# Optimization experiments

Measured on AMD Instinct MI355X. Metric: run time of the kernel, lower is better.

## Reference

```python
import jax, jax.numpy as jnp
import numpy as np

EPS = 1e-5
H = 12  # num_heads

def ste_sign(x):
    # forward: sign(x) in {-1,+1}; backward: grad passes where |x|<1 (clip STE)
    c = jnp.clip(x, -1.0, 1.0)
    s = jnp.where(x >= 0, 1.0, -1.0).astype(x.dtype)
    return c + jax.lax.stop_gradient(s - c)

def bin_w(w):
    # adaptive per-output-channel scaling: alpha = mean|w| (detached), weight = alpha*sign(w)
    alpha = jax.lax.stop_gradient(jnp.mean(jnp.abs(w), axis=1, keepdims=True))
    return alpha * ste_sign(w)

def layernorm(x, g, b):
    mu = jnp.mean(x, axis=-1, keepdims=True)
    var = jnp.var(x, axis=-1, keepdims=True)
    return (x - mu) * jax.lax.rsqrt(var + EPS) * g + b

def setup_inputs():
    key = jax.random.key(0)
    ks = jax.random.split(key, 6)
    B, N, C, hid = 8, 1024, 768, 3072
    s = 0.02
    return {
        "x": jax.random.normal(ks[0], (B, N, C), jnp.float32),
        "ln1_g": jnp.ones((C,), jnp.float32),
        "ln1_b": jnp.zeros((C,), jnp.float32),
        "w_qkv": jax.random.normal(ks[1], (3 * C, C), jnp.float32) * s,
        "w_proj": jax.random.normal(ks[2], (C, C), jnp.float32) * s,
        "b_proj": jnp.zeros((C,), jnp.float32),
        "ls1_g": 1e-5 * jnp.ones((C,), jnp.float32),
        "ln2_g": jnp.ones((C,), jnp.float32),
        "ln2_b": jnp.zeros((C,), jnp.float32),
        "w_fc1": jax.random.normal(ks[3], (hid, C), jnp.float32) * s,
        "b_fc1": jnp.zeros((hid,), jnp.float32),
        "w_fc2": jax.random.normal(ks[4], (C, hid), jnp.float32) * s,
        "b_fc2": jnp.zeros((C,), jnp.float32),
        "ls2_g": 1e-5 * jnp.ones((C,), jnp.float32),
    }

def reference(x, ln1_g, ln1_b, w_qkv, w_proj, b_proj, ls1_g, ln2_g, ln2_b, w_fc1, b_fc1, w_fc2, b_fc2, ls2_g):
    B, N, C = x.shape
    hd = C // H
    scale = hd ** -0.5
    # --- binarized attention ---
    h = layernorm(x, ln1_g, ln1_b)
    qkv = jnp.einsum('bnc,oc->bno', ste_sign(h), bin_w(w_qkv))        # 1w1a qkv proj
    qkv = qkv.reshape(B, N, 3, H, hd).transpose(2, 0, 3, 1, 4)        # [3,B,H,N,hd]
    bqkv = ste_sign(qkv)                                              # BinaryQuantizer
    q, k, v = bqkv[0], bqkv[1], bqkv[2]
    attn = jnp.einsum('bhnd,bhmd->bhnm', q, k) * scale                # [B,H,N,N]
    sm = jax.nn.softmax(attn, axis=-1)
    abin = (attn > 0).astype(x.dtype)                                 # SoftmaxBinaryQuantizer fwd value
    attn_eff = sm + jax.lax.stop_gradient(abin - sm)                  # STE: fwd=binary, bwd=softmax
    o = jnp.einsum('bhnm,bhmd->bhnd', attn_eff, v)
    o = o.transpose(0, 2, 1, 3).reshape(B, N, C)
    o = jnp.einsum('bnc,oc->bno', ste_sign(o), bin_w(w_proj)) + b_proj
    x = x + ls1_g * o
    # --- binary MLP (1-bit weight, 32-bit activation) ---
    h2 = layernorm(x, ln2_g, ln2_b)
    m = jax.nn.gelu(jnp.einsum('bnc,hc->bnh', h2, bin_w(w_fc1)) + b_fc1, approximate=False)
    m = jnp.einsum('bnh,ch->bnc', m, bin_w(w_fc2)) + b_fc2
    return x + ls2_g * m
```

## Files before the change

kernel.cpp:

```cpp
#include <hip/hip_runtime.h>

#define NTOK 8192
#define CDIM 768
#define HIDD 3072
#define NQKV 2304
#define SEQL 1024
#define NHEAD 12

typedef int i32x4 __attribute__((ext_vector_type(4)));
typedef float f32x4 __attribute__((ext_vector_type(4)));
typedef signed char sc16 __attribute__((ext_vector_type(16)));
typedef unsigned short us4 __attribute__((ext_vector_type(4)));

__device__ __forceinline__ unsigned short f32_to_bf16(float f) {
    unsigned int u = __float_as_uint(f);
    u += 0x7FFFu + ((u >> 16) & 1u);
    return (unsigned short)(u >> 16);
}
__device__ __forceinline__ float bf16_to_f32(unsigned short h) {
    return __uint_as_float(((unsigned)h) << 16);
}

__device__ __forceinline__ void gload_lds16(const void* g, void* l) {
    __builtin_amdgcn_global_load_lds(
        (const __attribute__((address_space(1))) unsigned int*)g,
        (__attribute__((address_space(3))) unsigned int*)l, 16, 0, 0);
}

__global__ void __launch_bounds__(256) prep_all(
    const float* __restrict__ w_proj, const float* __restrict__ w_fc1,
    const float* __restrict__ w_fc2,  const float* __restrict__ w_qkv,
    signed char* __restrict__ wproj_s, signed char* __restrict__ wfc1_s,
    signed char* __restrict__ wfc2_s,  signed char* __restrict__ wqkv_s,
    float* __restrict__ a_proj, float* __restrict__ a_fc1, float* __restrict__ a_fc2,
    const float* __restrict__ x, const float* __restrict__ ln1_g,
    const float* __restrict__ ln1_b, signed char* __restrict__ a1)
{
    const int blk = blockIdx.x;
    __shared__ float red[8];

    if (blk >= 6912) {
        int row = blk - 6912;
        const float* xr = x + (size_t)row * CDIM;
        float v0 = xr[threadIdx.x], v1 = xr[threadIdx.x + 256], v2 = xr[threadIdx.x + 512];
        float s = v0 + v1 + v2, s2 = v0 * v0 + v1 * v1 + v2 * v2;
        for (int off = 32; off > 0; off >>= 1) { s += __shfl_down(s, off); s2 += __shfl_down(s2, off); }
        if ((threadIdx.x & 63) == 0) { red[threadIdx.x >> 6] = s; red[4 + (threadIdx.x >> 6)] = s2; }
        __syncthreads();
        float ts = red[0] + red[1] + red[2] + red[3];
        float t2 = red[4] + red[5] + red[6] + red[7];
        float mu = ts * (1.0f / CDIM);
        float var = t2 * (1.0f / CDIM) - mu * mu;
        float rstd = rsqrtf(var + 1e-5f);
        signed char* orow = a1 + (size_t)row * CDIM;
        float vv[3] = {v0, v1, v2};
#pragma unroll
        for (int p = 0; p < 3; p++) {
            int i = threadIdx.x + p * 256;
            float val = (vv[p] - mu) * rstd * ln1_g[i] + ln1_b[i];
            orow[i] = (val >= 0.f) ? 1 : -1;
        }
        return;
    }

    const float* w; signed char* ws; float* alpha; int K; bool perm; int row;
    if (blk < 768)       { w = w_proj; ws = wproj_s; alpha = a_proj; K = CDIM; perm = true;  row = blk; }
    else if (blk < 3840) { w = w_fc1;  ws = wfc1_s;  alpha = a_fc1;  K = CDIM; perm = false; row = blk - 768; }
    else if (blk < 4608) { w = w_fc2;  ws = wfc2_s;  alpha = a_fc2;  K = HIDD; perm = true;  row = blk - 3840; }
    else                 { w = w_qkv;  ws = wqkv_s;  alpha = nullptr; K = CDIM; perm = false; row = blk - 4608; }

    const float* wr = w + (size_t)row * K;
    signed char* wsr = ws + (size_t)row * K;
    float s = 0.f;
    for (int i = threadIdx.x; i < K; i += 256) {
        float v = wr[i];
        int ip = perm ? ((i & ~63) | (((i & 15) << 2) | ((i >> 4) & 3))) : i;
        wsr[ip] = (v >= 0.f) ? 1 : -1;
        s += fabsf(v);
    }
    if (alpha) {
        for (int off = 32; off > 0; off >>= 1) s += __shfl_down(s, off);
        if ((threadIdx.x & 63) == 0) red[threadIdx.x >> 6] = s;
        __syncthreads();
        if (threadIdx.x == 0) alpha[row] = (red[0] + red[1] + red[2] + red[3]) / (float)K;
    }
}

__global__ void __launch_bounds__(256) ln2q_kernel(const unsigned short* __restrict__ x, const float* __restrict__ g,
                                                   const float* __restrict__ b, signed char* __restrict__ out,
                                                   float* __restrict__ rowscale) {
    int row = blockIdx.x;
    const unsigned short* xr = x + (size_t)row * CDIM;
    float v0 = bf16_to_f32(xr[threadIdx.x]);
    float v1 = bf16_to_f32(xr[threadIdx.x + 256]);
    float v2 = bf16_to_f32(xr[threadIdx.x + 512]);
    float s = v0 + v1 + v2, s2 = v0 * v0 + v1 * v1 + v2 * v2;
    for (int off = 32; off > 0; off >>= 1) { s += __shfl_down(s, off); s2 += __shfl_down(s2, off); }
    __shared__ float red[8];
    __shared__ float redm[4];
    if ((threadIdx.x & 63) == 0) { red[threadIdx.x >> 6] = s; red[4 + (threadIdx.x >> 6)] = s2; }
    __syncthreads();
    float ts = red[0] + red[1] + red[2] + red[3];
    float t2 = red[4] + red[5] + red[6] + red[7];
    float mu = ts * (1.0f / CDIM);
    float var = t2 * (1.0f / CDIM) - mu * mu;
    float rstd = rsqrtf(var + 1e-5f);
    float a0 = (v0 - mu) * rstd * g[threadIdx.x] + b[threadIdx.x];
    float a1 = (v1 - mu) * rstd * g[threadIdx.x + 256] + b[threadIdx.x + 256];
    float a2v = (v2 - mu) * rstd * g[threadIdx.x + 512] + b[threadIdx.x + 512];
    float mx = fmaxf(fabsf(a0), fmaxf(fabsf(a1), fabsf(a2v)));
    for (int off = 32; off > 0; off >>= 1) mx = fmaxf(mx, __shfl_down(mx, off));
    if ((threadIdx.x & 63) == 0) redm[threadIdx.x >> 6] = mx;
    __syncthreads();
    float rmax = fmaxf(fmaxf(redm[0], redm[1]), fmaxf(redm[2], redm[3]));
    rmax = fmaxf(rmax, 1e-20f);
    float inv = 127.f / rmax;
    signed char* orow = out + (size_t)row * CDIM;
    orow[threadIdx.x]       = (signed char)__float2int_rn(a0 * inv);
    orow[threadIdx.x + 256] = (signed char)__float2int_rn(a1 * inv);
    orow[threadIdx.x + 512] = (signed char)__float2int_rn(a2v * inv);
    if (threadIdx.x == 0) rowscale[row] = rmax * (1.f / 127.f);
}

enum { EPI_GELU = 2, EPI_QKV = 3 };
#define MSCALE_INV 16.0f

template<int EPI>
__global__ void __launch_bounds__(512, 4) gemm_i8(
    const signed char* __restrict__ A, const signed char* __restrict__ B,
    int M, int N, int K,
    const float* __restrict__ alpha, const float* __restrict__ bias,
    const float* __restrict__ rowscale,
    signed char* __restrict__ outB, signed char* __restrict__ vtB)
{
    __shared__ __align__(16) char lds_raw[3 * (256 + 128) * 64];
    auto As = (signed char (*)[256][64])lds_raw;
    auto Bs = (signed char (*)[128][64])(lds_raw + 3 * 256 * 64);

    const int tid = threadIdx.x, ln = tid & 63, w = tid >> 6;
    const int wm = w >> 1, wn = w & 1;
    const int lq = ln & 15, khi = ln >> 4;

    const int nwg = gridDim.x * gridDim.y;
    const int id = blockIdx.y * gridDim.x + blockIdx.x;
    const int nid = (id & 7) * (nwg >> 3) + (id >> 3);
    const int bxs = nid % gridDim.x, bys = nid / gridDim.x;
    const int bm = bys * 256, bn = bxs * 128;

    const i32x4 iz = {0, 0, 0, 0};
    i32x4 acc[4][4];
#pragma unroll
    for (int m = 0; m < 4; m++)
#pragma unroll
        for (int n = 0; n < 4; n++) acc[m][n] = iz;

    const int srow = tid >> 2, scol = (tid & 3) * 16;
    const int ssrc = ((tid & 3) ^ ((srow >> 1) & 3)) * 16;
    const int sa = 16 * (khi ^ ((lq >> 1) & 3));

    auto STAGE = [&](int p, int k0) {
        gload_lds16(A + (size_t)(bm + srow) * K + k0 + ssrc, &As[p][srow][scol]);
        gload_lds16(A + (size_t)(bm + 128 + srow) * K + k0 + ssrc, &As[p][128 + srow][scol]);
        gload_lds16(B + (size_t)(bn + srow) * K + k0 + ssrc, &Bs[p][srow][scol]);
    };
    auto COMPUTE = [&](int p, bool prefetch, int knext) {
        i32x4 aF[4], bF[4];
#pragma unroll
        for (int m = 0; m < 4; m++) aF[m] = *(const i32x4*)&As[p][wm * 64 + m * 16 + lq][sa];
#pragma unroll
        for (int n = 0; n < 4; n++) bF[n] = *(const i32x4*)&Bs[p][wn * 64 + n * 16 + lq][sa];
        if (prefetch) STAGE((p + 2) % 3, knext);
        __builtin_amdgcn_s_setprio(1);
#pragma unroll
        for (int m = 0; m < 4; m++)
#pragma unroll
            for (int n = 0; n < 4; n++)
                acc[m][n] = __builtin_amdgcn_mfma_i32_16x16x64_i8(aF[m], bF[n], acc[m][n], 0, 0, 0);
        __builtin_amdgcn_s_setprio(0);
    };

    const int nst = K >> 6;
    STAGE(0, 0);
    STAGE(1, 64);
#pragma unroll 1
    for (int t = 0; t < nst - 1; t++) {
        asm volatile("s_waitcnt vmcnt(3)" ::: "memory");
        asm volatile("s_waitcnt lgkmcnt(0)" ::: "memory");
        __builtin_amdgcn_s_barrier();
        COMPUTE(t % 3, t + 2 < nst, (t + 2) << 6);
    }
    asm volatile("s_waitcnt vmcnt(0)" ::: "memory");
    asm volatile("s_waitcnt lgkmcnt(0)" ::: "memory");
    __builtin_amdgcn_s_barrier();
    COMPUTE((nst - 1) % 3, false, 0);

    const int r0 = bm + wm * 64;
    const int c0 = bn + wn * 64;

    if constexpr (EPI == EPI_GELU) {
        float al[4], bi[4];
#pragma unroll
        for (int n = 0; n < 4; n++) {
            al[n] = alpha[c0 + n * 16 + lq];
            bi[n] = bias[c0 + n * 16 + lq];
        }
#pragma unroll
        for (int m = 0; m < 4; m++)
#pragma unroll
            for (int i = 0; i < 4; i++) {
                int r = r0 + m * 16 + khi * 4 + i;
                float rs = rowscale[r];
                unsigned pk = 0;
#pragma unroll
                for (int n = 0; n < 4; n++) {
                    float t = al[n] * ((float)acc[m][n][i] * rs) + bi[n];
                    float y2 = 1.5957691f * t + 0.07135481f * t * t * t;
                    float ge = t * __builtin_amdgcn_rcpf(1.0f + __expf(-y2));
                    float qf = fminf(fmaxf(ge * MSCALE_INV, -127.f), 127.f);
                    pk |= (unsigned)(unsigned char)(signed char)__float2int_rn(qf) << (8 * n);
                }
                *(unsigned*)(outB + (size_t)r * N + c0 + lq * 4) = pk;
            }
    } else {
        if (c0 < 1536) {
#pragma unroll
            for (int m = 0; m < 4; m++)
#pragma unroll
                for (int i = 0; i < 4; i++) {
                    int r = r0 + m * 16 + khi * 4 + i;
                    unsigned pk = 0;
#pragma unroll
                    for (int n = 0; n < 4; n++)
                        pk |= (unsigned)(unsigned char)(signed char)((acc[m][n][i] >= 0) ? 1 : -1) << (8 * n);
                    *(unsigned*)(outB + (size_t)r * 1536 + c0 + lq * 4) = pk;
                }
        } else {
#pragma unroll
            for (int m = 0; m < 4; m++)
#pragma unroll
                for (int n = 0; n < 4; n++) {
                    int cg = c0 + n * 16 + lq - 1536;
                    int hh = cg >> 6, dd = cg & 63;
                    int rb = r0 + m * 16 + khi * 4;
                    unsigned pk = 0;
#pragma unroll
                    for (int i = 0; i < 4; i++)
                        pk |= (unsigned)(unsigned char)(signed char)((acc[m][n][i] >= 0) ? 1 : -1) << (8 * i);
                    *(unsigned*)(vtB + (((size_t)(rb >> 10) * NHEAD + hh) * 64 + dd) * SEQL + (rb & 1023)) = pk;
                }
        }
    }
}

template<bool FINAL>
__global__ void __launch_bounds__(256) gemm_resid(
    const signed char* __restrict__ A, const signed char* __restrict__ B,
    int N, int K,
    const float* __restrict__ alpha, const float* __restrict__ bias,
    const float* __restrict__ ls,
    const float* __restrict__ residF, const unsigned short* __restrict__ residH,
    float ascale,
    float* __restrict__ outF, unsigned short* __restrict__ outH)
{
    __shared__ __align__(16) char lds_raw[3 * (128 + 64) * 64];
    auto As = (signed char (*)[128][64])lds_raw;
    auto Bs = (signed char (*)[64][64])(lds_raw + 3 * 128 * 64);

    const int tid = threadIdx.x, ln = tid & 63, w = tid >> 6;
    const int wm = w >> 1, wn = w & 1;
    const int lq = ln & 15, khi = ln >> 4;

    const int nwg = gridDim.x * gridDim.y;
    const int id = blockIdx.y * gridDim.x + blockIdx.x;
    const int nid = (id & 7) * (nwg >> 3) + (id >> 3);
    const int bxs = nid % gridDim.x, bys = nid / gridDim.x;
    const int bm = bys * 128, bn = bxs * 64;

    const int erow = tid >> 4;
    const int ec4 = (tid & 15) * 4;
    f32x4 a4 = *(const f32x4*)&alpha[bn + ec4];
    f32x4 b4 = *(const f32x4*)&bias[bn + ec4];
    f32x4 l4 = *(const f32x4*)&ls[bn + ec4];
    f32x4 rF[8];
    us4 rH[8];
#pragma unroll
    for (int p = 0; p < 8; p++) {
        size_t g = (size_t)(bm + p * 16 + erow) * N + bn + ec4;
        if constexpr (FINAL) rH[p] = *(const us4*)&residH[g];
        else                 rF[p] = *(const f32x4*)&residF[g];
    }

    const i32x4 iz = {0, 0, 0, 0};
    i32x4 acc[4][2];
#pragma unroll
    for (int m = 0; m < 4; m++)
#pragma unroll
        for (int n = 0; n < 2; n++) acc[m][n] = iz;

    const int srow = tid >> 2, scol = (tid & 3) * 16;
    const int ssrc = ((tid & 3) ^ ((srow >> 1) & 3)) * 16;
    const int sa = 16 * (khi ^ ((lq >> 1) & 3));

    auto STAGE = [&](int p, int k0) {
        gload_lds16(A + (size_t)(bm + srow) * K + k0 + ssrc, &As[p][srow][scol]);
        gload_lds16(A + (size_t)(bm + 64 + srow) * K + k0 + ssrc, &As[p][64 + srow][scol]);
        gload_lds16(B + (size_t)(bn + srow) * K + k0 + ssrc, &Bs[p][srow][scol]);
    };
    auto COMPUTE = [&](int p, bool prefetch, int knext) {
        i32x4 aF[4], bF[2];
#pragma unroll
        for (int m = 0; m < 4; m++) aF[m] = *(const i32x4*)&As[p][wm * 64 + m * 16 + lq][sa];
#pragma unroll
        for (int n = 0; n < 2; n++) bF[n] = *(const i32x4*)&Bs[p][wn * 32 + n * 16 + lq][sa];
        if (prefetch) STAGE((p + 2) % 3, knext);
        __builtin_amdgcn_s_setprio(1);
#pragma unroll
        for (int m = 0; m < 4; m++)
#pragma unroll
            for (int n = 0; n < 2; n++)
                acc[m][n] = __builtin_amdgcn_mfma_i32_16x16x64_i8(aF[m], bF[n], acc[m][n], 0, 0, 0);
        __builtin_amdgcn_s_setprio(0);
    };

    const int nst = K >> 6;
    STAGE(0, 0);
    STAGE(1, 64);
#pragma unroll 1
    for (int t = 0; t < nst - 1; t++) {
        asm volatile("s_waitcnt vmcnt(3)" ::: "memory");
        asm volatile("s_waitcnt lgkmcnt(0)" ::: "memory");
        __builtin_amdgcn_s_barrier();
        COMPUTE(t % 3, t + 2 < nst, (t + 2) << 6);
    }
    asm volatile("s_waitcnt vmcnt(0)" ::: "memory");
    asm volatile("s_waitcnt lgkmcnt(0)" ::: "memory");
    __builtin_amdgcn_s_barrier();
    COMPUTE((nst - 1) % 3, false, 0);

    __syncthreads();
    float (*Cf)[68] = (float (*)[68])lds_raw;
#pragma unroll
    for (int m = 0; m < 4; m++)
#pragma unroll
        for (int n = 0; n < 2; n++)
#pragma unroll
            for (int i = 0; i < 4; i++)
                Cf[wm * 64 + m * 16 + khi * 4 + i][wn * 32 + n * 16 + lq] =
                    (float)acc[m][n][i] * ascale;
    __syncthreads();
#pragma unroll
    for (int p = 0; p < 8; p++) {
        int row = p * 16 + erow;
        f32x4 v4 = *(const f32x4*)&Cf[row][ec4];
        size_t g = (size_t)(bm + row) * N + bn + ec4;
        if constexpr (FINAL) {
            f32x4 r;
            r.x = bf16_to_f32(rH[p].x); r.y = bf16_to_f32(rH[p].y);
            r.z = bf16_to_f32(rH[p].z); r.w = bf16_to_f32(rH[p].w);
            f32x4 o4 = r + l4 * (a4 * v4 + b4);
            *(f32x4*)&outF[g] = o4;
        } else {
            f32x4 o4 = rF[p] + l4 * (a4 * v4 + b4);
            us4 h;
            h.x = f32_to_bf16(o4.x); h.y = f32_to_bf16(o4.y);
            h.z = f32_to_bf16(o4.z); h.w = f32_to_bf16(o4.w);
            *(us4*)&outH[g] = h;
        }
    }
}

__global__ void __launch_bounds__(256) attn_v2(const signed char* __restrict__ qk,
                                               const signed char* __restrict__ vt,
                                               signed char* __restrict__ a2) {
    const int id = blockIdx.x;
    const int nid = (id & 7) * 96 + (id >> 3);
    const int bh = nid >> 3, qb = nid & 7;
    const int b = bh / NHEAD, h = bh % NHEAD;
    const int tid = threadIdx.x, ln = tid & 63, w = tid >> 6;
    const int lq = ln & 15, khi = ln >> 4;

    __shared__ signed char Ks[64][80];
    __shared__ signed char Vts[64][80];
    __shared__ signed char Pw[4][32][80];

    const size_t tokbase = (size_t)b * SEQL;
    const int q0 = qb * 128 + w * 32;
    const int str = tid >> 2, stc = (tid & 3) * 16;
    const size_t vtrow = ((size_t)bh * 64 + str) * SEQL;

    i32x4 qfrag[2];
#pragma unroll
    for (int qf = 0; qf < 2; qf++)
        qfrag[qf] = *(const i32x4*)(qk + (tokbase + q0 + qf * 16 + lq) * 1536 + h * 64 + khi * 16);

    const i32x4 iz = {0, 0, 0, 0};
    i32x4 o[2][4];
#pragma unroll
    for (int qf = 0; qf < 2; qf++)
#pragma unroll
        for (int df = 0; df < 4; df++) o[qf][df] = iz;

    auto LOADJ = [&](int j, sc16& kr, sc16& vr) {
        kr = *(const sc16*)(qk + (tokbase + j * 64 + str) * 1536 + 768 + h * 64 + stc);
        vr = *(const sc16*)(vt + vtrow + j * 64 + stc);
    };
    auto STORE = [&](const sc16& kr, const sc16& vr) {
        *(sc16*)&Ks[str][stc] = kr;
        *(sc16*)&Vts[str][stc] = vr;
    };
    auto COMPUTE = [&]() {
        i32x4 kfrag[4];
#pragma unroll
        for (int kf = 0; kf < 4; kf++)
            kfrag[kf] = *(const i32x4*)&Ks[kf * 16 + lq][khi * 16];
#pragma unroll
        for (int kf = 0; kf < 4; kf++) {
#pragma unroll
            for (int qf = 0; qf < 2; qf++) {
                i32x4 st = __builtin_amdgcn_mfma_i32_16x16x64_i8(kfrag[kf], qfrag[qf], iz, 0, 0, 0);
                unsigned pb = (st[0] > 0 ? 1u : 0u) | (st[1] > 0 ? 0x100u : 0u) |
                              (st[2] > 0 ? 0x10000u : 0u) | (st[3] > 0 ? 0x1000000u : 0u);
                *(unsigned*)&Pw[w][qf * 16 + lq][kf * 16 + khi * 4] = pb;
            }
        }
        i32x4 pa[2];
#pragma unroll
        for (int qf = 0; qf < 2; qf++)
            pa[qf] = *(const i32x4*)&Pw[w][qf * 16 + lq][khi * 16];
#pragma unroll
        for (int df = 0; df < 4; df++) {
            i32x4 vfr = *(const i32x4*)&Vts[df * 16 + lq][khi * 16];
#pragma unroll
            for (int qf = 0; qf < 2; qf++)
                o[qf][df] = __builtin_amdgcn_mfma_i32_16x16x64_i8(pa[qf], vfr, o[qf][df], 0, 0, 0);
        }
    };

    sc16 ka, va, kb, vb;
    LOADJ(0, ka, va);
#pragma unroll 1
    for (int jj = 0; jj < 16; jj += 2) {
        __syncthreads();
        STORE(ka, va);
        __syncthreads();
        LOADJ(jj + 1, kb, vb);
        COMPUTE();
        __syncthreads();
        STORE(kb, vb);
        __syncthreads();
        if (jj + 2 < 16) LOADJ(jj + 2, ka, va);
        COMPUTE();
    }

#pragma unroll
    for (int qf = 0; qf < 2; qf++)
#pragma unroll
        for (int i = 0; i < 4; i++) {
            int qrow = q0 + qf * 16 + khi * 4 + i;
            unsigned pk = 0;
#pragma unroll
            for (int df = 0; df < 4; df++)
                pk |= (unsigned)(unsigned char)(signed char)((o[qf][df][i] >= 0) ? 1 : -1) << (8 * df);
            *(unsigned*)(a2 + (tokbase + qrow) * CDIM + h * 64 + lq * 4) = pk;
        }
}

static const size_t OFF_WQKV  = 0;
static const size_t OFF_WPROJ = 1769472;
static const size_t OFF_WFC1  = 2359296;
static const size_t OFF_WFC2  = 4718592;
static const size_t OFF_APROJ = 7077888;
static const size_t OFF_AFC1  = 7080960;
static const size_t OFF_AFC2  = 7093248;
static const size_t OFF_H2SC  = 7096320;
static const size_t OFF_QK    = 7129088;
static const size_t OFF_VT    = 19712000;
static const size_t OFF_A1    = 26003456;
static const size_t OFF_A2    = 32294912;
static const size_t OFF_M1    = 38586368;
static const size_t OFF_H2    = 63752192;
static const size_t OFF_X1B   = OFF_QK;

extern "C" void kernel_launch(void* const* d_in, const int* in_sizes, int n_in,
                              void* d_out, int out_size, void* d_ws, size_t ws_size,
                              hipStream_t stream) {
    const float* x      = (const float*)d_in[0];
    const float* ln1_g  = (const float*)d_in[1];
    const float* ln1_b  = (const float*)d_in[2];
    const float* w_qkv  = (const float*)d_in[3];
    const float* w_proj = (const float*)d_in[4];
    const float* b_proj = (const float*)d_in[5];
    const float* ls1_g  = (const float*)d_in[6];
    const float* ln2_g  = (const float*)d_in[7];
    const float* ln2_b  = (const float*)d_in[8];
    const float* w_fc1  = (const float*)d_in[9];
    const float* b_fc1  = (const float*)d_in[10];
    const float* w_fc2  = (const float*)d_in[11];
    const float* b_fc2  = (const float*)d_in[12];
    const float* ls2_g  = (const float*)d_in[13];
    float* out = (float*)d_out;

    char* ws = (char*)d_ws;
    signed char* wqkv_s  = (signed char*)(ws + OFF_WQKV);
    signed char* wproj_s = (signed char*)(ws + OFF_WPROJ);
    signed char* wfc1_s  = (signed char*)(ws + OFF_WFC1);
    signed char* wfc2_s  = (signed char*)(ws + OFF_WFC2);
    float* a_proj  = (float*)(ws + OFF_APROJ);
    float* a_fc1   = (float*)(ws + OFF_AFC1);
    float* a_fc2   = (float*)(ws + OFF_AFC2);
    float* h2scale = (float*)(ws + OFF_H2SC);
    signed char* qk   = (signed char*)(ws + OFF_QK);
    signed char* vt   = (signed char*)(ws + OFF_VT);
    signed char* a1   = (signed char*)(ws + OFF_A1);
    signed char* a2   = (signed char*)(ws + OFF_A2);
    signed char* m1   = (signed char*)(ws + OFF_M1);
    signed char* h2   = (signed char*)(ws + OFF_H2);
    unsigned short* x1b = (unsigned short*)(ws + OFF_X1B);

    prep_all<<<15104, 256, 0, stream>>>(
        w_proj, w_fc1, w_fc2, w_qkv,
        wproj_s, wfc1_s, wfc2_s, wqkv_s,
        a_proj, a_fc1, a_fc2,
        x, ln1_g, ln1_b, a1);

    gemm_i8<EPI_QKV><<<dim3(NQKV / 128, NTOK / 256), 512, 0, stream>>>(
        a1, wqkv_s, NTOK, NQKV, CDIM, nullptr, nullptr, nullptr, qk, vt);

    attn_v2<<<768, 256, 0, stream>>>(qk, vt, a2);

    gemm_resid<false><<<dim3(CDIM / 64, NTOK / 128), 256, 0, stream>>>(
        a2, wproj_s, CDIM, CDIM, a_proj, b_proj, ls1_g, x, nullptr, 1.0f, nullptr, x1b);

    ln2q_kernel<<<NTOK, 256, 0, stream>>>(x1b, ln2_g, ln2_b, h2, h2scale);

    gemm_i8<EPI_GELU><<<dim3(HIDD / 128, NTOK / 256), 512, 0, stream>>>(
        h2, wfc1_s, NTOK, HIDD, CDIM, a_fc1, b_fc1, h2scale, m1, nullptr);

    gemm_resid<true><<<dim3(CDIM / 64, NTOK / 128), 256, 0, stream>>>(
        m1, wfc2_s, CDIM, HIDD, a_fc2, b_fc2, ls2_g, nullptr, x1b, 1.0f / MSCALE_INV, out, nullptr);
}
```

Baseline: 157.5 us.

## Split weight prep and overlap proj/fc weight binarization with attention

Weight binarization is split. Only the QKV weights are signed together with LN1 before the QKV GEMM. The proj/fc1/fc2 sign+alpha work moves into extra blocks of the attention kernel so it can fill idle CUs alongside the 768 attention blocks. The first residual is also written as bf16 in the prep pass, so the proj GEMM reads a half-size residual instead of fp32. This removes a separate prep bottleneck and some residual bandwidth, at the cost of bf16 rounding on the first residual and possible interference with attention blocks.

```diff
diff --git a/kernel.cpp b/kernel.cpp
--- a/kernel.cpp
+++ b/kernel.cpp
@@ -27,48 +27,10 @@
         (__attribute__((address_space(3))) unsigned int*)l, 16, 0, 0);
 }
 
-__global__ void __launch_bounds__(256) prep_all(
-    const float* __restrict__ w_proj, const float* __restrict__ w_fc1,
-    const float* __restrict__ w_fc2,  const float* __restrict__ w_qkv,
-    signed char* __restrict__ wproj_s, signed char* __restrict__ wfc1_s,
-    signed char* __restrict__ wfc2_s,  signed char* __restrict__ wqkv_s,
-    float* __restrict__ a_proj, float* __restrict__ a_fc1, float* __restrict__ a_fc2,
-    const float* __restrict__ x, const float* __restrict__ ln1_g,
-    const float* __restrict__ ln1_b, signed char* __restrict__ a1)
+__device__ __forceinline__ void sign_alpha_row(
+    const float* __restrict__ w, signed char* __restrict__ ws,
+    float* __restrict__ alpha, int K, bool perm, int row, float* red)
 {
-    const int blk = blockIdx.x;
-    __shared__ float red[8];
-
-    if (blk >= 6912) {
-        int row = blk - 6912;
-        const float* xr = x + (size_t)row * CDIM;
-        float v0 = xr[threadIdx.x], v1 = xr[threadIdx.x + 256], v2 = xr[threadIdx.x + 512];
-        float s = v0 + v1 + v2, s2 = v0 * v0 + v1 * v1 + v2 * v2;
-        for (int off = 32; off > 0; off >>= 1) { s += __shfl_down(s, off); s2 += __shfl_down(s2, off); }
-        if ((threadIdx.x & 63) == 0) { red[threadIdx.x >> 6] = s; red[4 + (threadIdx.x >> 6)] = s2; }
-        __syncthreads();
-        float ts = red[0] + red[1] + red[2] + red[3];
-        float t2 = red[4] + red[5] + red[6] + red[7];
-        float mu = ts * (1.0f / CDIM);
-        float var = t2 * (1.0f / CDIM) - mu * mu;
-        float rstd = rsqrtf(var + 1e-5f);
-        signed char* orow = a1 + (size_t)row * CDIM;
-        float vv[3] = {v0, v1, v2};
-#pragma unroll
-        for (int p = 0; p < 3; p++) {
-            int i = threadIdx.x + p * 256;
-            float val = (vv[p] - mu) * rstd * ln1_g[i] + ln1_b[i];
-            orow[i] = (val >= 0.f) ? 1 : -1;
-        }
-        return;
-    }
-
-    const float* w; signed char* ws; float* alpha; int K; bool perm; int row;
-    if (blk < 768)       { w = w_proj; ws = wproj_s; alpha = a_proj; K = CDIM; perm = true;  row = blk; }
-    else if (blk < 3840) { w = w_fc1;  ws = wfc1_s;  alpha = a_fc1;  K = CDIM; perm = false; row = blk - 768; }
-    else if (blk < 4608) { w = w_fc2;  ws = wfc2_s;  alpha = a_fc2;  K = HIDD; perm = true;  row = blk - 3840; }
-    else                 { w = w_qkv;  ws = wqkv_s;  alpha = nullptr; K = CDIM; perm = false; row = blk - 4608; }
-
     const float* wr = w + (size_t)row * K;
     signed char* wsr = ws + (size_t)row * K;
     float s = 0.f;
@@ -83,6 +45,45 @@
         if ((threadIdx.x & 63) == 0) red[threadIdx.x >> 6] = s;
         __syncthreads();
         if (threadIdx.x == 0) alpha[row] = (red[0] + red[1] + red[2] + red[3]) / (float)K;
+    }
+}
+
+__global__ void __launch_bounds__(256) prep_front(
+    const float* __restrict__ w_qkv, signed char* __restrict__ wqkv_s,
+    const float* __restrict__ x, const float* __restrict__ ln1_g,
+    const float* __restrict__ ln1_b, signed char* __restrict__ a1,
+    unsigned short* __restrict__ xb16)
+{
+    const int blk = blockIdx.x;
+    __shared__ float red[8];
+
+    if (blk < 2304) {
+        sign_alpha_row(w_qkv, wqkv_s, nullptr, CDIM, false, blk, red);
+        return;
+    }
+    int row = blk - 2304;
+    const float* xr = x + (size_t)row * CDIM;
+    float v0 = xr[threadIdx.x], v1 = xr[threadIdx.x + 256], v2 = xr[threadIdx.x + 512];
+    unsigned short* xbrow = xb16 + (size_t)row * CDIM;
+    xbrow[threadIdx.x]       = f32_to_bf16(v0);
+    xbrow[threadIdx.x + 256] = f32_to_bf16(v1);
+    xbrow[threadIdx.x + 512] = f32_to_bf16(v2);
+    float s = v0 + v1 + v2, s2 = v0 * v0 + v1 * v1 + v2 * v2;
+    for (int off = 32; off > 0; off >>= 1) { s += __shfl_down(s, off); s2 += __shfl_down(s2, off); }
+    if ((threadIdx.x & 63) == 0) { red[threadIdx.x >> 6] = s; red[4 + (threadIdx.x >> 6)] = s2; }
+    __syncthreads();
+    float ts = red[0] + red[1] + red[2] + red[3];
+    float t2 = red[4] + red[5] + red[6] + red[7];
+    float mu = ts * (1.0f / CDIM);
+    float var = t2 * (1.0f / CDIM) - mu * mu;
+    float rstd = rsqrtf(var + 1e-5f);
+    signed char* orow = a1 + (size_t)row * CDIM;
+    float vv[3] = {v0, v1, v2};
+#pragma unroll
+    for (int p = 0; p < 3; p++) {
+        int i = threadIdx.x + p * 256;
+        float val = (vv[p] - mu) * rstd * ln1_g[i] + ln1_b[i];
+        orow[i] = (val >= 0.f) ? 1 : -1;
     }
 }
 
@@ -252,13 +253,12 @@
     }
 }
 
-template<bool FINAL>
+template<bool OUTF32>
 __global__ void __launch_bounds__(256) gemm_resid(
     const signed char* __restrict__ A, const signed char* __restrict__ B,
     int N, int K,
     const float* __restrict__ alpha, const float* __restrict__ bias,
-    const float* __restrict__ ls,
-    const float* __restrict__ residF, const unsigned short* __restrict__ residH,
+    const float* __restrict__ ls, const unsigned short* __restrict__ residH,
     float ascale,
     float* __restrict__ outF, unsigned short* __restrict__ outH)
 {
@@ -281,13 +281,11 @@
     f32x4 a4 = *(const f32x4*)&alpha[bn + ec4];
     f32x4 b4 = *(const f32x4*)&bias[bn + ec4];
     f32x4 l4 = *(const f32x4*)&ls[bn + ec4];
-    f32x4 rF[8];
     us4 rH[8];
 #pragma unroll
     for (int p = 0; p < 8; p++) {
         size_t g = (size_t)(bm + p * 16 + erow) * N + bn + ec4;
-        if constexpr (FINAL) rH[p] = *(const us4*)&residH[g];
-        else                 rF[p] = *(const f32x4*)&residF[g];
+        rH[p] = *(const us4*)&residH[g];
     }
 
     const i32x4 iz = {0, 0, 0, 0};
@@ -353,14 +351,13 @@
         int row = p * 16 + erow;
         f32x4 v4 = *(const f32x4*)&Cf[row][ec4];
         size_t g = (size_t)(bm + row) * N + bn + ec4;
-        if constexpr (FINAL) {
-            f32x4 r;
-            r.x = bf16_to_f32(rH[p].x); r.y = bf16_to_f32(rH[p].y);
-            r.z = bf16_to_f32(rH[p].z); r.w = bf16_to_f32(rH[p].w);
-            f32x4 o4 = r + l4 * (a4 * v4 + b4);
+        f32x4 r;
+        r.x = bf16_to_f32(rH[p].x); r.y = bf16_to_f32(rH[p].y);
+        r.z = bf16_to_f32(rH[p].z); r.w = bf16_to_f32(rH[p].w);
+        f32x4 o4 = r + l4 * (a4 * v4 + b4);
+        if constexpr (OUTF32) {
             *(f32x4*)&outF[g] = o4;
         } else {
-            f32x4 o4 = rF[p] + l4 * (a4 * v4 + b4);
             us4 h;
             h.x = f32_to_bf16(o4.x); h.y = f32_to_bf16(o4.y);
             h.z = f32_to_bf16(o4.z); h.w = f32_to_bf16(o4.w);
@@ -369,10 +366,25 @@
     }
 }
 
-__global__ void __launch_bounds__(256) attn_v2(const signed char* __restrict__ qk,
-                                               const signed char* __restrict__ vt,
-                                               signed char* __restrict__ a2) {
-    const int id = blockIdx.x;
+__global__ void __launch_bounds__(256) attn_prep(
+    const signed char* __restrict__ qk, const signed char* __restrict__ vt,
+    signed char* __restrict__ a2,
+    const float* __restrict__ w_proj, const float* __restrict__ w_fc1,
+    const float* __restrict__ w_fc2,
+    signed char* __restrict__ wproj_s, signed char* __restrict__ wfc1_s,
+    signed char* __restrict__ wfc2_s,
+    float* __restrict__ a_proj, float* __restrict__ a_fc1, float* __restrict__ a_fc2)
+{
+    const int blk = blockIdx.x;
+    if (blk >= 768) {
+        __shared__ float red[4];
+        if (blk < 1536)      sign_alpha_row(w_proj, wproj_s, a_proj, CDIM, true,  blk - 768, red);
+        else if (blk < 4608) sign_alpha_row(w_fc1,  wfc1_s,  a_fc1,  CDIM, false, blk - 1536, red);
+        else                 sign_alpha_row(w_fc2,  wfc2_s,  a_fc2,  HIDD, true,  blk - 4608, red);
+        return;
+    }
+
+    const int id = blk;
     const int nid = (id & 7) * 96 + (id >> 3);
     const int bh = nid >> 3, qb = nid & 7;
     const int b = bh / NHEAD, h = bh % NHEAD;
@@ -480,6 +492,7 @@
 static const size_t OFF_M1    = 38586368;
 static const size_t OFF_H2    = 63752192;
 static const size_t OFF_X1B   = OFF_QK;
+static const size_t OFF_XB16  = OFF_M1;
 
 extern "C" void kernel_launch(void* const* d_in, const int* in_sizes, int n_in,
                               void* d_out, int out_size, void* d_ws, size_t ws_size,
@@ -515,21 +528,21 @@
     signed char* a2   = (signed char*)(ws + OFF_A2);
     signed char* m1   = (signed char*)(ws + OFF_M1);
     signed char* h2   = (signed char*)(ws + OFF_H2);
-    unsigned short* x1b = (unsigned short*)(ws + OFF_X1B);
-
-    prep_all<<<15104, 256, 0, stream>>>(
-        w_proj, w_fc1, w_fc2, w_qkv,
-        wproj_s, wfc1_s, wfc2_s, wqkv_s,
-        a_proj, a_fc1, a_fc2,
-        x, ln1_g, ln1_b, a1);
+    unsigned short* x1b  = (unsigned short*)(ws + OFF_X1B);
+    unsigned short* xb16 = (unsigned short*)(ws + OFF_XB16);
+
+    prep_front<<<2304 + NTOK, 256, 0, stream>>>(w_qkv, wqkv_s, x, ln1_g, ln1_b, a1, xb16);
 
     gemm_i8<EPI_QKV><<<dim3(NQKV / 128, NTOK / 256), 512, 0, stream>>>(
         a1, wqkv_s, NTOK, NQKV, CDIM, nullptr, nullptr, nullptr, qk, vt);
 
-    attn_v2<<<768, 256, 0, stream>>>(qk, vt, a2);
+    attn_prep<<<5376, 256, 0, stream>>>(qk, vt, a2,
+                                        w_proj, w_fc1, w_fc2,
+                                        wproj_s, wfc1_s, wfc2_s,
+                                        a_proj, a_fc1, a_fc2);
 
     gemm_resid<false><<<dim3(CDIM / 64, NTOK / 128), 256, 0, stream>>>(
-        a2, wproj_s, CDIM, CDIM, a_proj, b_proj, ls1_g, x, nullptr, 1.0f, nullptr, x1b);
+        a2, wproj_s, CDIM, CDIM, a_proj, b_proj, ls1_g, xb16, 1.0f, nullptr, x1b);
 
     ln2q_kernel<<<NTOK, 256, 0, stream>>>(x1b, ln2_g, ln2_b, h2, h2scale);
 
@@ -537,5 +550,5 @@
         h2, wfc1_s, NTOK, HIDD, CDIM, a_fc1, b_fc1, h2scale, m1, nullptr);
 
     gemm_resid<true><<<dim3(CDIM / 64, NTOK / 128), 256, 0, stream>>>(
-        m1, wfc2_s, CDIM, HIDD, a_fc2, b_fc2, ls2_g, nullptr, x1b, 1.0f / MSCALE_INV, out, nullptr);
-}
+        m1, wfc2_s, CDIM, HIDD, a_fc2, b_fc2, ls2_g, x1b, 1.0f / MSCALE_INV, out, nullptr);
+}
```

Result: no change. 157.2 us (-0.2%).
